# Optimization experiments

Hardware: AMD Instinct MI355X
Metric: run time of the kernel (lower is better)

## Reference

```python
import jax, jax.numpy as jnp
import numpy as np

DIM = 512
NUM_HEADS = 8
HEAD_SIZE = 64
INNER = NUM_HEADS * HEAD_SIZE  # 512


def setup_inputs() -> dict:
    key = jax.random.key(0)
    k1, k2, k3, k4, k5 = jax.random.split(key, 5)
    x = jax.random.normal(k1, (2, 4096, DIM), dtype=jnp.float32)
    # Linear params stored as [in, out] for y = x @ W + b (same math as torch Linear)
    w_qkv = jax.random.normal(k2, (DIM, INNER * 3), dtype=jnp.float32) * (1.0 / np.sqrt(DIM))
    b_qkv = jax.random.normal(k3, (INNER * 3,), dtype=jnp.float32) * 0.01
    w_out = jax.random.normal(k4, (INNER, DIM), dtype=jnp.float32) * (1.0 / np.sqrt(INNER))
    b_out = jax.random.normal(k5, (DIM,), dtype=jnp.float32) * 0.01
    return {"x": x, "w_qkv": w_qkv, "b_qkv": b_qkv, "w_out": w_out, "b_out": b_out}


def reference(x, w_qkv, b_qkv, w_out, b_out):
    b, n, _ = x.shape
    qkv = x @ w_qkv + b_qkv                      # [b, n, 3*inner]
    q, k, v = jnp.split(qkv, 3, axis=-1)          # each [b, n, inner]

    def heads(t):  # 'b n (h d) -> b h n d'
        return t.reshape(b, n, NUM_HEADS, HEAD_SIZE).transpose(0, 2, 1, 3)

    q, k, v = heads(q), heads(k), heads(v)
    scores = jnp.einsum('bhnd,bhmd->bhnm', q, k) / jnp.sqrt(jnp.float32(HEAD_SIZE))
    probs = jax.nn.softmax(scores, axis=-1)       # dropout is identity in eval
    out = jnp.einsum('bhnm,bhmd->bhnd', probs, v)
    out = out.transpose(0, 2, 1, 3).reshape(b, n, INNER)  # 'b h n d -> b n (h d)'
    return out @ w_out + b_out
```

## Files before the change

kernel.cpp:

```cpp
#include <hip/hip_runtime.h>

typedef __bf16 bf16;
typedef __bf16 bf16x8 __attribute__((ext_vector_type(8)));
typedef float f32x4 __attribute__((ext_vector_type(4)));

#define MFMA16(a, b, c) __builtin_amdgcn_mfma_f32_16x16x32_bf16((a), (b), (c), 0, 0, 0)

static __device__ __forceinline__ bf16x8 ldg8(const bf16* p) {
  return *(const bf16x8*)p;
}


__global__ __launch_bounds__(256) void cvt_pack_x(const float* __restrict__ x,
                                                  bf16* __restrict__ Xp) {
  int mt = blockIdx.x, kc = blockIdx.y;
  int row = threadIdx.x >> 4;
  int c4 = (threadIdx.x & 15) * 4;
  bf16* tile = Xp + ((size_t)mt * 8 + kc) * 4096;
#pragma unroll
  for (int i = 0; i < 4; i++) {
    int r = i * 16 + row;
    const float* src = x + (size_t)(mt * 64 + r) * 512 + kc * 64 + c4;
    float4 v = *(const float4*)src;
    bf16* d = tile + r * 64 + c4;
    d[0] = (bf16)v.x; d[1] = (bf16)v.y; d[2] = (bf16)v.z; d[3] = (bf16)v.w;
  }
}

__global__ __launch_bounds__(256) void transpose_pack_w(const float* __restrict__ W,
                                                        bf16* __restrict__ Wp,
                                                        int N, int KC) {
  __shared__ bf16 tile[64][65];
  int kc = blockIdx.x, nt = blockIdx.y;
  int c = threadIdx.x & 63;
  int r4 = threadIdx.x >> 6;
#pragma unroll
  for (int i = 0; i < 16; i++) {
    int r = r4 * 16 + i;
    tile[r][c] = (bf16)W[(size_t)(kc * 64 + r) * N + nt * 64 + c];
  }
  __syncthreads();
  bf16* dst = Wp + ((size_t)nt * KC + kc) * 4096;
#pragma unroll
  for (int i = 0; i < 16; i++) {
    int r = r4 * 16 + i;
    dst[r * 64 + c] = tile[c][r];
  }
}

__device__ __forceinline__ void gemm_core_packed(const bf16* __restrict__ Ap,
                                                 const bf16* __restrict__ Bp,
                                                 int KC, bf16* Atile, bf16* Btile,
                                                 int tid, int wave, int l16,
                                                 int quad, f32x4 acc[4]) {
  for (int kc = 0; kc < KC; kc++) {
    __syncthreads();
    const bf16* ag = Ap + (size_t)kc * 4096;
    const bf16* bg = Bp + (size_t)kc * 4096;
#pragma unroll
    for (int rnd = 0; rnd < 2; rnd++) {
      int e = (rnd * 256 + tid) * 8;
      int row = e >> 6;
      int c16 = (e & 63) >> 3;
      int unit = row * 8 + (c16 ^ (row & 7));
      *(bf16x8*)&Atile[unit * 8] = ldg8(ag + e);
      *(bf16x8*)&Btile[unit * 8] = ldg8(bg + e);
    }
    __syncthreads();

    int ar = wave * 16 + l16;
    bf16x8 a0 = *(const bf16x8*)&Atile[(ar * 8 + (quad ^ (ar & 7))) * 8];
    bf16x8 a1 = *(const bf16x8*)&Atile[(ar * 8 + ((4 + quad) ^ (ar & 7))) * 8];
#pragma unroll
    for (int ct = 0; ct < 4; ct++) {
      int n = ct * 16 + l16;
      bf16x8 b0 = *(const bf16x8*)&Btile[(n * 8 + (quad ^ (n & 7))) * 8];
      bf16x8 b1 = *(const bf16x8*)&Btile[(n * 8 + ((4 + quad) ^ (n & 7))) * 8];
      acc[ct] = MFMA16(a0, b0, acc[ct]);
      acc[ct] = MFMA16(a1, b1, acc[ct]);
    }
  }
}

__global__ __launch_bounds__(256) void qkv_gemm(const bf16* __restrict__ Xp,
                                                const bf16* __restrict__ Wp1,
                                                const float* __restrict__ bqkv,
                                                bf16* __restrict__ Q,
                                                bf16* __restrict__ Kh,
                                                bf16* __restrict__ Vt) {
  int mt = blockIdx.x, nt = blockIdx.y;
  int tid = threadIdx.x;
  int wave = tid >> 6, lane = tid & 63;
  int l16 = lane & 15, quad = lane >> 4;

  __shared__ __align__(16) bf16 Atile[4096];
  __shared__ __align__(16) bf16 Btile[4096];

  f32x4 acc[4] = {};
  gemm_core_packed(Xp + (size_t)mt * 8 * 4096, Wp1 + (size_t)nt * 8 * 4096, 8,
                   Atile, Btile, tid, wave, l16, quad, acc);

#pragma unroll
  for (int ct = 0; ct < 4; ct++) {
    int c = nt * 64 + ct * 16 + l16;
    float bias = bqkv[c];
    int which = c >> 9, inner = c & 511;
    int h = inner >> 6, d = inner & 63;
#pragma unroll
    for (int r = 0; r < 4; r++) {
      int m = mt * 64 + wave * 16 + quad * 4 + r;
      int b = m >> 12, n = m & 4095;
      int bh = b * 8 + h;
      float v = acc[ct][r] + bias;
      if (which == 0)
        Q[((size_t)bh * 4096 + n) * 64 + d] = (bf16)(v * 0.125f);
      else if (which == 1)
        Kh[((size_t)bh * 4096 + n) * 64 + d] = (bf16)v;
      else
        Vt[(((size_t)bh * 64 + (n >> 6)) * 64 + d) * 64 + (n & 63)] = (bf16)v;
    }
  }
}

__global__ __launch_bounds__(256, 4) void flash_partial(const bf16* __restrict__ Q,
                                                        const bf16* __restrict__ K,
                                                        const bf16* __restrict__ Vt,
                                                        bf16* __restrict__ Opart,
                                                        float* __restrict__ Lpart) {
  int strip = blockIdx.x, bh = blockIdx.y, half = blockIdx.z;
  int tid = threadIdx.x;
  int wave = tid >> 6, lane = tid & 63;
  int l16 = lane & 15, quad = lane >> 4;

  const bf16* Qh = Q + (size_t)bh * 4096 * 64;
  const bf16* Kg = K + ((size_t)bh * 4096 + half * 2048) * 64;
  const bf16* Vg = Vt + (size_t)bh * 64 * 4096 + (size_t)half * 2048 * 64;

  __shared__ __align__(16) bf16 Klds[4096];
  __shared__ __align__(16) bf16 Vlds[4096];
  __shared__ __align__(16) bf16 P[4][32][72];

  int qbase = strip * 128 + wave * 32;
  bf16x8 aq[2][2];
#pragma unroll
  for (int mt = 0; mt < 2; mt++) {
    const bf16* qr = Qh + (size_t)(qbase + mt * 16 + l16) * 64;
    aq[mt][0] = ldg8(qr + quad * 8);
    aq[mt][1] = ldg8(qr + 32 + quad * 8);
  }

  f32x4 o[2][4] = {};
  float l_lane[2][4] = {};

  int e0 = tid * 8, e1 = (256 + tid) * 8;
  int r0 = e0 >> 6, r1 = e1 >> 6;
  int u0 = r0 * 8 + (((e0 & 63) >> 3) ^ (r0 & 7));
  int u1 = r1 * 8 + (((e1 & 63) >> 3) ^ (r1 & 7));

  bf16x8 kp0 = ldg8(Kg + e0), kp1 = ldg8(Kg + e1);
  bf16x8 vp0 = ldg8(Vg + e0), vp1 = ldg8(Vg + e1);

  for (int kb = 0; kb < 2048; kb += 64) {
    __syncthreads();
    *(bf16x8*)&Klds[u0 * 8] = kp0;
    *(bf16x8*)&Klds[u1 * 8] = kp1;
    *(bf16x8*)&Vlds[u0 * 8] = vp0;
    *(bf16x8*)&Vlds[u1 * 8] = vp1;
    __syncthreads();

    if (kb + 64 < 2048) {
      const bf16* kg = Kg + (size_t)(kb + 64) * 64;
      const bf16* vg = Vg + (size_t)(kb + 64) * 64;
      kp0 = ldg8(kg + e0);
      kp1 = ldg8(kg + e1);
      vp0 = ldg8(vg + e0);
      vp1 = ldg8(vg + e1);
    }

    f32x4 s[2][4] = {};
#pragma unroll
    for (int ct = 0; ct < 4; ct++) {
      int n = ct * 16 + l16;
      bf16x8 b0 = *(const bf16x8*)&Klds[(n * 8 + (quad ^ (n & 7))) * 8];
      bf16x8 b1 = *(const bf16x8*)&Klds[(n * 8 + ((4 + quad) ^ (n & 7))) * 8];
#pragma unroll
      for (int mt = 0; mt < 2; mt++) {
        s[mt][ct] = MFMA16(aq[mt][0], b0, s[mt][ct]);
        s[mt][ct] = MFMA16(aq[mt][1], b1, s[mt][ct]);
      }
    }
#pragma unroll
    for (int mt = 0; mt < 2; mt++)
#pragma unroll
      for (int ct = 0; ct < 4; ct++)
#pragma unroll
        for (int r = 0; r < 4; r++) {
          float p = __expf(s[mt][ct][r]);
          l_lane[mt][r] += p;
          P[wave][mt * 16 + quad * 4 + r][ct * 16 + l16] = (bf16)p;
        }
#pragma unroll
    for (int mt = 0; mt < 2; mt++) {
      bf16x8 ap0 = ldg8(&P[wave][mt * 16 + l16][quad * 8]);
      bf16x8 ap1 = ldg8(&P[wave][mt * 16 + l16][32 + quad * 8]);
#pragma unroll
      for (int ct = 0; ct < 4; ct++) {
        int d = ct * 16 + l16;
        bf16x8 bv0 = *(const bf16x8*)&Vlds[(d * 8 + (quad ^ (d & 7))) * 8];
        bf16x8 bv1 = *(const bf16x8*)&Vlds[(d * 8 + ((4 + quad) ^ (d & 7))) * 8];
        o[mt][ct] = MFMA16(ap0, bv0, o[mt][ct]);
        o[mt][ct] = MFMA16(ap1, bv1, o[mt][ct]);
      }
    }
  }

  size_t u = ((size_t)half * 16 + bh) * 32 + strip;
  bf16* op = Opart + u * 8192;
#pragma unroll
  for (int mt = 0; mt < 2; mt++) {
    float lrow[4];
#pragma unroll
    for (int r = 0; r < 4; r++) {
      float l = l_lane[mt][r];
#pragma unroll
      for (int off = 1; off < 16; off <<= 1) l += __shfl_xor(l, off);
      lrow[r] = l;
    }
#pragma unroll
    for (int ct = 0; ct < 4; ct++)
#pragma unroll
      for (int r = 0; r < 4; r++)
        op[(wave * 32 + mt * 16 + quad * 4 + r) * 64 + ct * 16 + l16] =
            (bf16)o[mt][ct][r];
    if (l16 == 0) {
#pragma unroll
      for (int r = 0; r < 4; r++)
        Lpart[u * 128 + wave * 32 + mt * 16 + quad * 4 + r] = lrow[r];
    }
  }
}

__global__ __launch_bounds__(256) void flash_combine(const bf16* __restrict__ Opart,
                                                     const float* __restrict__ Lpart,
                                                     bf16* __restrict__ Ap) {
  int qt = blockIdx.x, bh = blockIdx.y;
  int col = threadIdx.x & 63;
  int rg = threadIdx.x >> 6;
  int strip = qt >> 1;
  int rbase = (qt & 1) * 64;
  size_t u0 = (size_t)bh * 32 + strip;
  size_t u1 = ((size_t)16 + bh) * 32 + strip;
  int b = bh >> 3, h = bh & 7;
  bf16* apt = Ap + (((size_t)(b * 64 + qt)) * 8 + h) * 4096;
#pragma unroll
  for (int i = 0; i < 16; i++) {
    int r64 = rg * 16 + i;
    int row = rbase + r64;
    float o0 = (float)Opart[u0 * 8192 + row * 64 + col];
    float o1 = (float)Opart[u1 * 8192 + row * 64 + col];
    float ls = Lpart[u0 * 128 + row] + Lpart[u1 * 128 + row];
    apt[r64 * 64 + col] = (bf16)((o0 + o1) / ls);
  }
}

__global__ __launch_bounds__(256) void out_gemm(const bf16* __restrict__ Ap,
                                                const bf16* __restrict__ Wp2,
                                                const float* __restrict__ bout,
                                                float* __restrict__ Out) {
  int mt = blockIdx.x, nt = blockIdx.y;
  int tid = threadIdx.x;
  int wave = tid >> 6, lane = tid & 63;
  int l16 = lane & 15, quad = lane >> 4;

  __shared__ __align__(16) bf16 Atile[4096];
  __shared__ __align__(16) bf16 Btile[4096];

  f32x4 acc[4] = {};
  gemm_core_packed(Ap + (size_t)mt * 8 * 4096, Wp2 + (size_t)nt * 8 * 4096, 8,
                   Atile, Btile, tid, wave, l16, quad, acc);

#pragma unroll
  for (int ct = 0; ct < 4; ct++) {
    int c = nt * 64 + ct * 16 + l16;
    float bias = bout[c];
#pragma unroll
    for (int r = 0; r < 4; r++) {
      int m = mt * 64 + wave * 16 + quad * 4 + r;
      Out[(size_t)m * 512 + c] = acc[ct][r] + bias;
    }
  }
}

extern "C" void kernel_launch(void* const* d_in, const int* in_sizes, int n_in,
                              void* d_out, int out_size, void* d_ws,
                              size_t ws_size, hipStream_t stream) {
  const float* x = (const float*)d_in[0];
  const float* w_qkv = (const float*)d_in[1];
  const float* b_qkv = (const float*)d_in[2];
  const float* w_out = (const float*)d_in[3];
  const float* b_out = (const float*)d_in[4];
  float* out = (float*)d_out;

  char* ws = (char*)d_ws;
  bf16* Q = (bf16*)(ws + 0);
  bf16* K = (bf16*)(ws + 8388608);
  bf16* Vt = (bf16*)(ws + 16777216);
  bf16* Ap = (bf16*)(ws + 25165824);
  bf16* Wp1 = (bf16*)(ws + 33554432);
  bf16* Wp2 = (bf16*)(ws + 35127296);
  bf16* Xp = (bf16*)(ws + 35651584);
  bf16* Opart = (bf16*)(ws + 44040192);
  float* Lpart = (float*)(ws + 60817408);

  cvt_pack_x<<<dim3(128, 8), 256, 0, stream>>>(x, Xp);
  transpose_pack_w<<<dim3(8, 24), 256, 0, stream>>>(w_qkv, Wp1, 1536, 8);
  transpose_pack_w<<<dim3(8, 8), 256, 0, stream>>>(w_out, Wp2, 512, 8);
  qkv_gemm<<<dim3(128, 24), 256, 0, stream>>>(Xp, Wp1, b_qkv, Q, K, Vt);
  flash_partial<<<dim3(32, 16, 2), 256, 0, stream>>>(Q, K, Vt, Opart, Lpart);
  flash_combine<<<dim3(64, 16), 256, 0, stream>>>(Opart, Lpart, Ap);
  out_gemm<<<dim3(128, 8), 256, 0, stream>>>(Ap, Wp2, b_out, out);
}
```

Baseline: 221.0 us.

## Keep attention probabilities in registers via transposed QK and permlane swaps

The flash partial kernel now computes S transposed (K as the A operand), so each lane holds the probabilities in an order that can be packed with v_cvt_pk_bf16 and rearranged with permlane32/16 swaps straight into the A-operand layout for the PV MFMA. This removes the per-wave LDS round trip for P. K/V tiles are double-buffered in LDS, which drops one barrier per iteration. s_setprio hints are placed around the MFMA sections. The cost is more LDS for the K/V buffers and a more intricate lane mapping that must match the MFMA layout exactly.

```diff
diff --git a/kernel.cpp b/kernel.cpp
--- a/kernel.cpp
+++ b/kernel.cpp
@@ -8,6 +8,17 @@
 
 static __device__ __forceinline__ bf16x8 ldg8(const bf16* p) {
   return *(const bf16x8*)p;
+}
+static __device__ __forceinline__ unsigned cvt_pk_bf16(float lo, float hi) {
+  unsigned d;
+  asm("v_cvt_pk_bf16_f32 %0, %1, %2" : "=v"(d) : "v"(lo), "v"(hi));
+  return d;
+}
+static __device__ __forceinline__ void pl32_swap(unsigned& a, unsigned& b) {
+  asm("v_permlane32_swap_b32 %0, %1" : "+v"(a), "+v"(b));
+}
+static __device__ __forceinline__ void pl16_swap(unsigned& a, unsigned& b) {
+  asm("v_permlane16_swap_b32 %0, %1" : "+v"(a), "+v"(b));
 }
 
 
@@ -136,9 +147,8 @@
   const bf16* Kg = K + ((size_t)bh * 4096 + half * 2048) * 64;
   const bf16* Vg = Vt + (size_t)bh * 64 * 4096 + (size_t)half * 2048 * 64;
 
-  __shared__ __align__(16) bf16 Klds[4096];
-  __shared__ __align__(16) bf16 Vlds[4096];
-  __shared__ __align__(16) bf16 P[4][32][72];
+  __shared__ __align__(16) bf16 Klds[2][4096];
+  __shared__ __align__(16) bf16 Vlds[2][4096];
 
   int qbase = strip * 128 + wave * 32;
   bf16x8 aq[2][2];
@@ -150,7 +160,7 @@
   }
 
   f32x4 o[2][4] = {};
-  float l_lane[2][4] = {};
+  float l_lane[2] = {0.f, 0.f};
 
   int e0 = tid * 8, e1 = (256 + tid) * 8;
   int r0 = e0 >> 6, r1 = e1 >> 6;
@@ -160,83 +170,101 @@
   bf16x8 kp0 = ldg8(Kg + e0), kp1 = ldg8(Kg + e1);
   bf16x8 vp0 = ldg8(Vg + e0), vp1 = ldg8(Vg + e1);
 
-  for (int kb = 0; kb < 2048; kb += 64) {
+#pragma unroll 2
+  for (int t = 0; t < 32; t++) {
+    int cur = t & 1;
+    bf16* kl = Klds[cur];
+    bf16* vl = Vlds[cur];
+    *(bf16x8*)&kl[u0 * 8] = kp0;
+    *(bf16x8*)&kl[u1 * 8] = kp1;
+    *(bf16x8*)&vl[u0 * 8] = vp0;
+    *(bf16x8*)&vl[u1 * 8] = vp1;
     __syncthreads();
-    *(bf16x8*)&Klds[u0 * 8] = kp0;
-    *(bf16x8*)&Klds[u1 * 8] = kp1;
-    *(bf16x8*)&Vlds[u0 * 8] = vp0;
-    *(bf16x8*)&Vlds[u1 * 8] = vp1;
-    __syncthreads();
-
-    if (kb + 64 < 2048) {
-      const bf16* kg = Kg + (size_t)(kb + 64) * 64;
-      const bf16* vg = Vg + (size_t)(kb + 64) * 64;
+
+    if (t < 31) {
+      const bf16* kg = Kg + (size_t)(t + 1) * 4096;
+      const bf16* vg = Vg + (size_t)(t + 1) * 4096;
       kp0 = ldg8(kg + e0);
       kp1 = ldg8(kg + e1);
       vp0 = ldg8(vg + e0);
       vp1 = ldg8(vg + e1);
     }
 
-    f32x4 s[2][4] = {};
-#pragma unroll
-    for (int ct = 0; ct < 4; ct++) {
-      int n = ct * 16 + l16;
-      bf16x8 b0 = *(const bf16x8*)&Klds[(n * 8 + (quad ^ (n & 7))) * 8];
-      bf16x8 b1 = *(const bf16x8*)&Klds[(n * 8 + ((4 + quad) ^ (n & 7))) * 8];
+#pragma unroll
+    for (int h2 = 0; h2 < 2; h2++) {
+      f32x4 s[2][2] = {};
+      __builtin_amdgcn_s_setprio(1);
+#pragma unroll
+      for (int c2 = 0; c2 < 2; c2++) {
+        int n = h2 * 32 + c2 * 16 + l16;
+        bf16x8 k0 = *(const bf16x8*)&kl[(n * 8 + (quad ^ (n & 7))) * 8];
+        bf16x8 k1 = *(const bf16x8*)&kl[(n * 8 + ((4 + quad) ^ (n & 7))) * 8];
+#pragma unroll
+        for (int mt = 0; mt < 2; mt++) {
+          s[mt][c2] = MFMA16(k0, aq[mt][0], s[mt][c2]);
+          s[mt][c2] = MFMA16(k1, aq[mt][1], s[mt][c2]);
+        }
+      }
+      __builtin_amdgcn_s_setprio(0);
+
+      bf16x8 pa[2];
 #pragma unroll
       for (int mt = 0; mt < 2; mt++) {
-        s[mt][ct] = MFMA16(aq[mt][0], b0, s[mt][ct]);
-        s[mt][ct] = MFMA16(aq[mt][1], b1, s[mt][ct]);
+        unsigned ue[2], wo[2];
+#pragma unroll
+        for (int c2 = 0; c2 < 2; c2++) {
+          float p0 = __expf(s[mt][c2][0]);
+          float p1 = __expf(s[mt][c2][1]);
+          float p2 = __expf(s[mt][c2][2]);
+          float p3 = __expf(s[mt][c2][3]);
+          l_lane[mt] += (p0 + p1) + (p2 + p3);
+          ue[c2] = cvt_pk_bf16(p0, p1);
+          wo[c2] = cvt_pk_bf16(p2, p3);
+        }
+        pl32_swap(ue[0], ue[1]);
+        pl16_swap(ue[0], ue[1]);
+        pl32_swap(wo[0], wo[1]);
+        pl16_swap(wo[0], wo[1]);
+        union { bf16x8 v; unsigned d[4]; } pk;
+        pk.d[0] = ue[0];
+        pk.d[1] = wo[0];
+        pk.d[2] = ue[1];
+        pk.d[3] = wo[1];
+        pa[mt] = pk.v;
       }
-    }
-#pragma unroll
-    for (int mt = 0; mt < 2; mt++)
-#pragma unroll
-      for (int ct = 0; ct < 4; ct++)
-#pragma unroll
-        for (int r = 0; r < 4; r++) {
-          float p = __expf(s[mt][ct][r]);
-          l_lane[mt][r] += p;
-          P[wave][mt * 16 + quad * 4 + r][ct * 16 + l16] = (bf16)p;
-        }
-#pragma unroll
-    for (int mt = 0; mt < 2; mt++) {
-      bf16x8 ap0 = ldg8(&P[wave][mt * 16 + l16][quad * 8]);
-      bf16x8 ap1 = ldg8(&P[wave][mt * 16 + l16][32 + quad * 8]);
+
+      __builtin_amdgcn_s_setprio(1);
 #pragma unroll
       for (int ct = 0; ct < 4; ct++) {
         int d = ct * 16 + l16;
-        bf16x8 bv0 = *(const bf16x8*)&Vlds[(d * 8 + (quad ^ (d & 7))) * 8];
-        bf16x8 bv1 = *(const bf16x8*)&Vlds[(d * 8 + ((4 + quad) ^ (d & 7))) * 8];
-        o[mt][ct] = MFMA16(ap0, bv0, o[mt][ct]);
-        o[mt][ct] = MFMA16(ap1, bv1, o[mt][ct]);
+        bf16x8 bv = *(const bf16x8*)&vl[(d * 8 + ((h2 * 4 + quad) ^ (d & 7))) * 8];
+        o[0][ct] = MFMA16(pa[0], bv, o[0][ct]);
+        o[1][ct] = MFMA16(pa[1], bv, o[1][ct]);
       }
-    }
-  }
-
-  size_t u = ((size_t)half * 16 + bh) * 32 + strip;
-  bf16* op = Opart + u * 8192;
+      __builtin_amdgcn_s_setprio(0);
+    }
+  }
+
+  float lf[2];
 #pragma unroll
   for (int mt = 0; mt < 2; mt++) {
-    float lrow[4];
-#pragma unroll
-    for (int r = 0; r < 4; r++) {
-      float l = l_lane[mt][r];
-#pragma unroll
-      for (int off = 1; off < 16; off <<= 1) l += __shfl_xor(l, off);
-      lrow[r] = l;
-    }
+    float l = l_lane[mt];
+    l += __shfl_xor(l, 16);
+    l += __shfl_xor(l, 32);
+    lf[mt] = l;
+  }
+  size_t ub = ((size_t)half * 16 + bh) * 32 + strip;
+  bf16* op = Opart + ub * 8192;
+#pragma unroll
+  for (int mt = 0; mt < 2; mt++) {
 #pragma unroll
     for (int ct = 0; ct < 4; ct++)
 #pragma unroll
       for (int r = 0; r < 4; r++)
         op[(wave * 32 + mt * 16 + quad * 4 + r) * 64 + ct * 16 + l16] =
             (bf16)o[mt][ct][r];
-    if (l16 == 0) {
-#pragma unroll
-      for (int r = 0; r < 4; r++)
-        Lpart[u * 128 + wave * 32 + mt * 16 + quad * 4 + r] = lrow[r];
-    }
+    if (quad == 0)
+      Lpart[ub * 128 + wave * 32 + mt * 16 + l16] = lf[mt];
   }
 }
 
```

After: 222.5 us. About the same (+0.7%).
